# Kernel tuning notes

Measured on AMD Instinct MI355X. Metric: run time of the kernel, lower is better.

## Reference

```python
import jax, jax.numpy as jnp
import numpy as np
from jax import lax

B, N = 16, 4096


def _fps(xyz, npoint):
    # xyz: [N,3] -> [npoint] int32 indices (iterative farthest point sampling, start at idx 0)
    n = xyz.shape[0]
    def step(carry, _):
        dist, far = carry
        d = jnp.sum((xyz - xyz[far]) ** 2, axis=-1)
        dist = jnp.minimum(dist, d)
        nxt = jnp.argmax(dist).astype(jnp.int32)
        return (dist, nxt), far
    (_, _), idx = lax.scan(step, (jnp.full((n,), 1e10, xyz.dtype), jnp.int32(0)), None, length=npoint)
    return idx


def _ball_query(xyz, new_xyz, radius, nsample):
    # xyz: [N,3], new_xyz: [S,3] -> [S, nsample] neighbor indices within radius
    n = xyz.shape[0]
    sqr = jnp.sum((new_xyz[:, None, :] - xyz[None, :, :]) ** 2, axis=-1)  # [S,N]
    idx = jnp.where(sqr > radius * radius, n, jnp.arange(n)[None, :])
    idx = jnp.sort(idx, axis=-1)[:, :nsample]
    return jnp.where(idx == n, idx[:, :1], idx)  # pad misses with first hit


def _gather(p, i):
    return p[i]


def _mlp(feat, ws):
    # feat: [B,S,K,C]; 1x1 conv + folded eval-BN + ReLU per layer
    for W, b in ws:
        feat = jax.nn.relu(jnp.einsum('bskc,oc->bsko', feat, W) + b)
    return feat


def _sa(xyz, points, npoint, radius, nsample, ws):
    fps_idx = jax.vmap(_fps, in_axes=(0, None))(xyz, npoint)              # [B,S]
    new_xyz = jnp.take_along_axis(xyz, fps_idx[..., None], axis=1)         # [B,S,3]
    idx = jax.vmap(_ball_query, in_axes=(0, 0, None, None))(xyz, new_xyz, radius, nsample)  # [B,S,K]
    grouped_xyz = jax.vmap(_gather)(xyz, idx) - new_xyz[:, :, None, :]     # [B,S,K,3]
    if points is None:
        feat = grouped_xyz
    else:
        feat = jnp.concatenate([grouped_xyz, jax.vmap(_gather)(points, idx)], axis=-1)
    return new_xyz, jnp.max(_mlp(feat, ws), axis=2)                        # [B,S,Cout]


def _forward(x, ws1, ws2, ws3, fw, fb):
    b = x.shape[0]
    l1_xyz, l1_pts = _sa(x, None, 512, 0.2, 32, ws1)       # [B,512,3], [B,512,128]
    l2_xyz, l2_pts = _sa(l1_xyz, l1_pts, 128, 0.4, 64, ws2)  # [B,128,3], [B,128,256]
    feat = jnp.concatenate([l2_xyz, l2_pts], axis=-1)[:, None]  # group_all: [B,1,128,259]
    g = jnp.max(_mlp(feat, ws3), axis=2).reshape(b, 1024)
    return g @ fw.T + fb


_SPECS = [
    ('sa1_w0', (64, 3)), ('sa1_b0', (64,)), ('sa1_w1', (64, 64)), ('sa1_b1', (64,)), ('sa1_w2', (128, 64)), ('sa1_b2', (128,)),
    ('sa2_w0', (128, 131)), ('sa2_b0', (128,)), ('sa2_w1', (128, 128)), ('sa2_b1', (128,)), ('sa2_w2', (256, 128)), ('sa2_b2', (256,)),
    ('sa3_w0', (256, 259)), ('sa3_b0', (256,)), ('sa3_w1', (512, 256)), ('sa3_b1', (512,)), ('sa3_w2', (1024, 512)), ('sa3_b2', (1024,)),
    ('fw', (1024, 1024)), ('fb', (1024,)),
]


def setup_inputs() -> dict:
    key = jax.random.key(0)
    keys = jax.random.split(key, len(_SPECS) + 1)
    inp = {'x': jax.random.uniform(keys[0], (B, N, 3), dtype=jnp.float32)}
    for (name, shp), k in zip(_SPECS, keys[1:]):
        inp[name] = jax.random.normal(k, shp, dtype=jnp.float32) * 0.02
    return inp


def reference(x, sa1_w0, sa1_b0, sa1_w1, sa1_b1, sa1_w2, sa1_b2,
              sa2_w0, sa2_b0, sa2_w1, sa2_b1, sa2_w2, sa2_b2,
              sa3_w0, sa3_b0, sa3_w1, sa3_b1, sa3_w2, sa3_b2, fw, fb):
    ws1 = [(sa1_w0, sa1_b0), (sa1_w1, sa1_b1), (sa1_w2, sa1_b2)]
    ws2 = [(sa2_w0, sa2_b0), (sa2_w1, sa2_b1), (sa2_w2, sa2_b2)]
    ws3 = [(sa3_w0, sa3_b0), (sa3_w1, sa3_b1), (sa3_w2, sa3_b2)]
    return _forward(x, ws1, ws2, ws3, fw, fb)
```

## Files before the change

### kernel.cpp

```cpp
#include <hip/hip_runtime.h>

#ifndef BATCH
#define BATCH 16
#endif

typedef float f32x2 __attribute__((ext_vector_type(2)));
__device__ __forceinline__ f32x2 mk2(float a, float b) { f32x2 r; r.x = a; r.y = b; return r; }

template<int CTRL>
__device__ __forceinline__ float dppmaxf(float v)
{
    const int d = __builtin_amdgcn_update_dpp(__float_as_int(v), __float_as_int(v),
                                              CTRL, 0xf, 0xf, false);
    return fmaxf(v, __int_as_float(d));
}
template<int CTRL>
__device__ __forceinline__ unsigned dppminu(unsigned v)
{
    const unsigned d = (unsigned)__builtin_amdgcn_update_dpp((int)v, (int)v,
                                                             CTRL, 0xf, 0xf, false);
    return (d < v) ? d : v;
}
__device__ __forceinline__ float wave_max_bcast(float v)
{
    v = dppmaxf<0x111>(v);
    v = dppmaxf<0x112>(v);
    v = dppmaxf<0x114>(v);
    v = dppmaxf<0x118>(v);
    v = dppmaxf<0x142>(v);
    v = dppmaxf<0x143>(v);
    return __int_as_float(__builtin_amdgcn_readlane(__float_as_int(v), 63));
}
__device__ __forceinline__ unsigned wave_min_bcast(unsigned v)
{
    v = dppminu<0x111>(v);
    v = dppminu<0x112>(v);
    v = dppminu<0x114>(v);
    v = dppminu<0x118>(v);
    v = dppminu<0x142>(v);
    v = dppminu<0x143>(v);
    return (unsigned)__builtin_amdgcn_readlane((int)v, 63);
}

__device__ __forceinline__ void transpose_body(int blk, int tid,
    const float* __restrict__ s0, float* __restrict__ d0,
    const float* __restrict__ s1, float* __restrict__ d1,
    const float* __restrict__ s2, float* __restrict__ d2,
    const float* __restrict__ s3, float* __restrict__ d3,
    const float* __restrict__ s4, float* __restrict__ d4,
    const float* __restrict__ s5, float* __restrict__ d5,
    const float* __restrict__ s6, float* __restrict__ d6,
    const float* __restrict__ s7, float* __restrict__ d7,
    const float* __restrict__ s8, float* __restrict__ d8)
{
    int i = blk * 256 + tid;
    if (i < 192)    { d0[(i%3)  *64   + i/3  ] = s0[i]; return; }  i -= 192;
    if (i < 4096)   { d1[(i&63) *64   + (i>>6)] = s1[i]; return; } i -= 4096;
    if (i < 8192)   { d2[(i&63) *128  + (i>>6)] = s2[i]; return; } i -= 8192;
    if (i < 16768)  { d3[(i%131)*128  + i/131] = s3[i]; return; }  i -= 16768;
    if (i < 16384)  { d4[(i&127)*128  + (i>>7)] = s4[i]; return; } i -= 16384;
    if (i < 32768)  { d5[(i&127)*256  + (i>>7)] = s5[i]; return; } i -= 32768;
    if (i < 66304)  { d6[(i%259)*256  + i/259] = s6[i]; return; }  i -= 66304;
    if (i < 131072) { d7[(i&255)*512  + (i>>8)] = s7[i]; return; } i -= 131072;
    if (i < 524288) { d8[(i&511)*1024 + (i>>9)] = s8[i]; return; }
}

template<int N, int NP1, int NP2, int BLOCK>
__global__ __launch_bounds__(BLOCK)
void fps_fused(const float* __restrict__ xyz,
               float* __restrict__ out1, float* __restrict__ out2,
               const float* __restrict__ ts0, float* __restrict__ td0,
               const float* __restrict__ ts1, float* __restrict__ td1,
               const float* __restrict__ ts2, float* __restrict__ td2,
               const float* __restrict__ ts3, float* __restrict__ td3,
               const float* __restrict__ ts4, float* __restrict__ td4,
               const float* __restrict__ ts5, float* __restrict__ td5,
               const float* __restrict__ ts6, float* __restrict__ td6,
               const float* __restrict__ ts7, float* __restrict__ td7,
               const float* __restrict__ ts8, float* __restrict__ td8)
{
#pragma clang fp contract(off)
    if ((int)blockIdx.x >= BATCH) {
        transpose_body(blockIdx.x - BATCH, threadIdx.x,
                       ts0, td0, ts1, td1, ts2, td2, ts3, td3, ts4, td4,
                       ts5, td5, ts6, td6, ts7, td7, ts8, td8);
        return;
    }
    constexpr int P  = N / BLOCK;
    constexpr int P2 = NP1 / BLOCK;
    constexpr int NW = BLOCK / 64;
    __shared__ float sx[N], sy[N], sz[N];
    __shared__ float s2x[NP1], s2y[NP1], s2z[NP1];
    __shared__ float o2x[NP2], o2y[NP2], o2z[NP2];
    __shared__ unsigned long long wslot[2][NW];
    const int b = blockIdx.x, t = threadIdx.x;
    const int lane = t & 63, wv = t >> 6;
    const float* xb = xyz + (size_t)b * N * 3;
    float px[P], py[P], pz[P], dist[P];
#pragma unroll
    for (int j = 0; j < P; ++j) {
        const int i = t + j * BLOCK;
        const float x = xb[i*3+0], y = xb[i*3+1], z = xb[i*3+2];
        sx[i] = x; sy[i] = y; sz[i] = z;
        px[j] = x; py[j] = y; pz[j] = z;
        dist[j] = 1e10f;
    }
    __syncthreads();
    float fx = sx[0], fy = sy[0], fz = sz[0];
    if (t == 0) { s2x[0] = fx; s2y[0] = fy; s2z[0] = fz; }
    for (int s = 1; s < NP1; ++s) {
        float bestv = -1.f; int besti = 0;
#pragma unroll
        for (int j = 0; j < P; ++j) {
            const float dx = px[j]-fx, dy = py[j]-fy, dz = pz[j]-fz;
            const float d = (dx*dx + dy*dy) + dz*dz;
            const float nd = fminf(dist[j], d);
            dist[j] = nd;
            if (nd > bestv) { bestv = nd; besti = t + j * BLOCK; }
        }
        const float wm = wave_max_bcast(bestv);
        const unsigned cand = (bestv == wm) ? (unsigned)besti : 0xffffffffu;
        const unsigned wi = wave_min_bcast(cand);
        const int par = s & 1;
        if (lane == 0)
            wslot[par][wv] = ((unsigned long long)__float_as_uint(wm) << 32)
                           | (unsigned)(~wi);
        __syncthreads();
        unsigned long long pa = wslot[par][0];
#pragma unroll
        for (int w = 1; w < NW; ++w) {
            const unsigned long long pb = wslot[par][w];
            pa = (pb > pa) ? pb : pa;
        }
        const int far = (int)(~(unsigned)pa);
        fx = sx[far]; fy = sy[far]; fz = sz[far];
        if (t == 0) { s2x[s] = fx; s2y[s] = fy; s2z[s] = fz; }
    }
    __syncthreads();
    float mx[P2], my[P2], mz[P2], d2[P2];
#pragma unroll
    for (int j = 0; j < P2; ++j) {
        const int i = t + j * BLOCK;
        mx[j] = s2x[i]; my[j] = s2y[i]; mz[j] = s2z[i];
        d2[j] = 1e10f;
    }
    fx = s2x[0]; fy = s2y[0]; fz = s2z[0];
    if (t == 0) { o2x[0] = fx; o2y[0] = fy; o2z[0] = fz; }
    for (int s = 1; s < NP2; ++s) {
        float bestv = -1.f; int besti = 0;
#pragma unroll
        for (int j = 0; j < P2; ++j) {
            const float dx = mx[j]-fx, dy = my[j]-fy, dz = mz[j]-fz;
            const float d = (dx*dx + dy*dy) + dz*dz;
            const float nd = fminf(d2[j], d);
            d2[j] = nd;
            if (nd > bestv) { bestv = nd; besti = t + j * BLOCK; }
        }
        const float wm = wave_max_bcast(bestv);
        const unsigned cand = (bestv == wm) ? (unsigned)besti : 0xffffffffu;
        const unsigned wi = wave_min_bcast(cand);
        const int par = s & 1;
        if (lane == 0)
            wslot[par][wv] = ((unsigned long long)__float_as_uint(wm) << 32)
                           | (unsigned)(~wi);
        __syncthreads();
        unsigned long long pa = wslot[par][0];
#pragma unroll
        for (int w = 1; w < NW; ++w) {
            const unsigned long long pb = wslot[par][w];
            pa = (pb > pa) ? pb : pa;
        }
        const int far2 = (int)(~(unsigned)pa);
        fx = s2x[far2]; fy = s2y[far2]; fz = s2z[far2];
        if (t == 0) { o2x[s] = fx; o2y[s] = fy; o2z[s] = fz; }
    }
    __syncthreads();
    for (int i = t; i < NP1; i += BLOCK) {
        out1[((size_t)b*NP1 + i)*3 + 0] = s2x[i];
        out1[((size_t)b*NP1 + i)*3 + 1] = s2y[i];
        out1[((size_t)b*NP1 + i)*3 + 2] = s2z[i];
    }
    for (int i = t; i < NP2; i += BLOCK) {
        out2[((size_t)b*NP2 + i)*3 + 0] = o2x[i];
        out2[((size_t)b*NP2 + i)*3 + 1] = o2y[i];
        out2[((size_t)b*NP2 + i)*3 + 2] = o2z[i];
    }
}

template<int N, int S, int K>
__device__ __forceinline__ void ballq_body(const float* __restrict__ xyz,
                                           const float* __restrict__ nxyz,
                                           int* __restrict__ idx, const float r2,
                                           const int bid, const int tid)
{
#pragma clang fp contract(off)
    const int gw = (bid * 256 + tid) >> 6;
    const int lane = tid & 63;
    const int b = gw / S, s = gw % S;
    const float* xb = xyz + (size_t)b * N * 3;
    const float qx = nxyz[((size_t)b*S + s)*3 + 0];
    const float qy = nxyz[((size_t)b*S + s)*3 + 1];
    const float qz = nxyz[((size_t)b*S + s)*3 + 2];
    int* op = idx + ((size_t)b*S + s) * K;
    int base = 0, first = -1;
    for (int c = 0; c < N; c += 64) {
        const int i = c + lane;
        const float dx = xb[i*3+0]-qx, dy = xb[i*3+1]-qy, dz = xb[i*3+2]-qz;
        const float d = (dx*dx + dy*dy) + dz*dz;
        const bool hit = !(d > r2);
        const unsigned long long m = __ballot(hit);
        if (first < 0 && m) first = c + __builtin_ctzll(m);
        const int pos = base + __popcll(m & ((1ull << lane) - 1ull));
        if (hit && pos < K) op[pos] = i;
        base += __popcll(m);
        if (base >= K) break;
    }
    if (base < K && lane >= base && lane < K) op[lane] = first;
}

__global__ __launch_bounds__(256)
void ballq_both(const float* __restrict__ pts1, const float* __restrict__ q1,
                int* __restrict__ idx1, const float r2a,
                const float* __restrict__ pts2, const float* __restrict__ q2,
                int* __restrict__ idx2, const float r2b)
{
    const int nb1 = (BATCH * 512) / 4;
    if ((int)blockIdx.x < nb1)
        ballq_body<4096, 512, 32>(pts1, q1, idx1, r2a, blockIdx.x, threadIdx.x);
    else
        ballq_body<512, 128, 64>(pts2, q2, idx2, r2b, blockIdx.x - nb1, threadIdx.x);
}

__device__ __forceinline__ void fma16pk(f32x2 (&acc)[8], const float f,
                                        const float* __restrict__ wrow)
{
    const float4 w0 = ((const float4*)wrow)[0];
    const float4 w1 = ((const float4*)wrow)[1];
    const float4 w2 = ((const float4*)wrow)[2];
    const float4 w3 = ((const float4*)wrow)[3];
    const f32x2 ff = mk2(f, f);
    acc[0] += ff * mk2(w0.x, w0.y);
    acc[1] += ff * mk2(w0.z, w0.w);
    acc[2] += ff * mk2(w1.x, w1.y);
    acc[3] += ff * mk2(w1.z, w1.w);
    acc[4] += ff * mk2(w2.x, w2.y);
    acc[5] += ff * mk2(w2.z, w2.w);
    acc[6] += ff * mk2(w3.x, w3.y);
    acc[7] += ff * mk2(w3.z, w3.w);
}

__device__ __forceinline__ float pool_half(float v)
{
    v = fmaxf(v, __shfl_xor(v, 1));
    v = fmaxf(v, __shfl_xor(v, 2));
    v = fmaxf(v, __shfl_xor(v, 4));
    v = fmaxf(v, __shfl_xor(v, 8));
    v = fmaxf(v, __shfl_xor(v, 16));
    return v;
}
__device__ __forceinline__ float pool_full(float v)
{
    v = pool_half(v);
    return fmaxf(v, __shfl_xor(v, 32));
}

__global__ __launch_bounds__(256)
void sa1_fused(const float* __restrict__ xyz, const float* __restrict__ nxyz,
               const int* __restrict__ idx,
               const float* __restrict__ Wt0, const float* __restrict__ B0,
               const float* __restrict__ Wt1, const float* __restrict__ B1,
               const float* __restrict__ Wt2, const float* __restrict__ B2,
               float* __restrict__ out)
{
    __shared__ float buf[64][64];
    const int tid = threadIdx.x, lane = tid & 63;
    const int wave = __builtin_amdgcn_readfirstlane(tid >> 6);
    const int row0 = blockIdx.x * 64;
    const int myrow = row0 + lane;
    const int g = myrow >> 5, b = g >> 9;
    const int i = idx[myrow];
    const float* p = xyz + ((size_t)b*4096 + i) * 3;
    const float f0 = p[0] - nxyz[(size_t)g*3 + 0];
    const float f1 = p[1] - nxyz[(size_t)g*3 + 1];
    const float f2 = p[2] - nxyz[(size_t)g*3 + 2];
    const int oc0 = wave * 16;
    f32x2 aL[8], aH[8];
#pragma unroll
    for (int j = 0; j < 16; ++j) {
        const float v = B0[oc0+j] + f0*Wt0[0*64+oc0+j] + f1*Wt0[1*64+oc0+j] + f2*Wt0[2*64+oc0+j];
        buf[oc0+j][lane] = fmaxf(v, 0.f);
    }
    __syncthreads();
#pragma unroll
    for (int k = 0; k < 8; ++k) aL[k] = mk2(B1[oc0+2*k], B1[oc0+2*k+1]);
#pragma unroll 4
    for (int ci = 0; ci < 64; ++ci)
        fma16pk(aL, buf[ci][lane], Wt1 + ci*64 + oc0);
    __syncthreads();
#pragma unroll
    for (int k = 0; k < 8; ++k) {
        buf[oc0+2*k][lane]   = fmaxf(aL[k].x, 0.f);
        buf[oc0+2*k+1][lane] = fmaxf(aL[k].y, 0.f);
    }
    __syncthreads();
#pragma unroll
    for (int k = 0; k < 8; ++k) {
        aL[k] = mk2(B2[oc0+2*k], B2[oc0+2*k+1]);
        aH[k] = mk2(B2[64+oc0+2*k], B2[64+oc0+2*k+1]);
    }
#pragma unroll 2
    for (int ci = 0; ci < 64; ++ci) {
        const float f = buf[ci][lane];
        fma16pk(aL, f, Wt2 + ci*128 + oc0);
        fma16pk(aH, f, Wt2 + ci*128 + 64 + oc0);
    }
#pragma unroll
    for (int k = 0; k < 8; ++k) {
        const float v0 = pool_half(fmaxf(aL[k].x, 0.f));
        const float v1 = pool_half(fmaxf(aL[k].y, 0.f));
        const float w0 = pool_half(fmaxf(aH[k].x, 0.f));
        const float w1 = pool_half(fmaxf(aH[k].y, 0.f));
        if ((lane & 31) == 0) {
            const size_t orow = (size_t)((row0 + lane) >> 5) * 128;
            out[orow + oc0 + 2*k]       = v0;
            out[orow + oc0 + 2*k + 1]   = v1;
            out[orow + 64 + oc0 + 2*k]     = w0;
            out[orow + 64 + oc0 + 2*k + 1] = w1;
        }
    }
}

__global__ __launch_bounds__(256)
void sa2_fused(const float* __restrict__ l1xyz, const float* __restrict__ l1pts,
               const float* __restrict__ nxyz, const int* __restrict__ idx,
               const float* __restrict__ Wt0, const float* __restrict__ B0,
               const float* __restrict__ Wt1, const float* __restrict__ B1,
               const float* __restrict__ Wt2, const float* __restrict__ B2,
               const float* __restrict__ Wt30, const float* __restrict__ B30,
               float* __restrict__ outH1)
{
    __shared__ float buf[128][64];
    __shared__ float pool[256];
    const int tid = threadIdx.x, lane = tid & 63;
    const int wave = __builtin_amdgcn_readfirstlane(tid >> 6);
    const int gblk = blockIdx.x;
    const int b = gblk >> 7;
    const int row0 = gblk * 64;
    const int myi = idx[row0 + lane];
    const float* pc = l1xyz + ((size_t)b*512 + myi) * 3;
    const float cx = nxyz[(size_t)gblk*3 + 0];
    const float cy = nxyz[(size_t)gblk*3 + 1];
    const float cz = nxyz[(size_t)gblk*3 + 2];
    const float f0 = pc[0] - cx;
    const float f1 = pc[1] - cy;
    const float f2 = pc[2] - cz;
    for (int r = wave; r < 64; r += 4) {
        const int i2 = idx[row0 + r];
        const float* src = l1pts + ((size_t)b*512 + i2) * 128;
        buf[lane][r ^ lane]    = src[lane];
        buf[lane+64][r ^ lane] = src[lane + 64];
    }
    __syncthreads();
    const int oc0 = wave * 16;
    f32x2 aL[8], aH[8];
#pragma unroll
    for (int k = 0; k < 8; ++k) {
        const int j0 = oc0 + 2*k, j1 = oc0 + 2*k + 1;
        aL[k] = mk2(B0[j0]    + f0*Wt0[j0]     + f1*Wt0[128+j0]    + f2*Wt0[256+j0],
                    B0[j1]    + f0*Wt0[j1]     + f1*Wt0[128+j1]    + f2*Wt0[256+j1]);
        aH[k] = mk2(B0[64+j0] + f0*Wt0[64+j0]  + f1*Wt0[192+j0]    + f2*Wt0[320+j0],
                    B0[64+j1] + f0*Wt0[64+j1]  + f1*Wt0[192+j1]    + f2*Wt0[320+j1]);
    }
#pragma unroll 2
    for (int ci = 0; ci < 128; ++ci) {
        const float f = buf[ci][lane ^ (ci & 63)];
        const float* wp = Wt0 + (size_t)(ci+3)*128;
        fma16pk(aL, f, wp + oc0);
        fma16pk(aH, f, wp + 64 + oc0);
    }
    __syncthreads();
#pragma unroll
    for (int k = 0; k < 8; ++k) {
        buf[oc0+2*k][lane]      = fmaxf(aL[k].x, 0.f);
        buf[oc0+2*k+1][lane]    = fmaxf(aL[k].y, 0.f);
        buf[64+oc0+2*k][lane]   = fmaxf(aH[k].x, 0.f);
        buf[64+oc0+2*k+1][lane] = fmaxf(aH[k].y, 0.f);
    }
    __syncthreads();
#pragma unroll
    for (int k = 0; k < 8; ++k) {
        aL[k] = mk2(B1[oc0+2*k], B1[oc0+2*k+1]);
        aH[k] = mk2(B1[64+oc0+2*k], B1[64+oc0+2*k+1]);
    }
#pragma unroll 2
    for (int ci = 0; ci < 128; ++ci) {
        const float f = buf[ci][lane];
        const float* wp = Wt1 + (size_t)ci*128;
        fma16pk(aL, f, wp + oc0);
        fma16pk(aH, f, wp + 64 + oc0);
    }
    __syncthreads();
#pragma unroll
    for (int k = 0; k < 8; ++k) {
        buf[oc0+2*k][lane]      = fmaxf(aL[k].x, 0.f);
        buf[oc0+2*k+1][lane]    = fmaxf(aL[k].y, 0.f);
        buf[64+oc0+2*k][lane]   = fmaxf(aH[k].x, 0.f);
        buf[64+oc0+2*k+1][lane] = fmaxf(aH[k].y, 0.f);
    }
    __syncthreads();
    for (int half = 0; half < 2; ++half) {
        const int oc = half*128 + oc0;
#pragma unroll
        for (int k = 0; k < 8; ++k) {
            aL[k] = mk2(B2[oc+2*k], B2[oc+2*k+1]);
            aH[k] = mk2(B2[64+oc+2*k], B2[64+oc+2*k+1]);
        }
#pragma unroll 2
        for (int ci = 0; ci < 128; ++ci) {
            const float f = buf[ci][lane];
            const float* wp = Wt2 + (size_t)ci*256;
            fma16pk(aL, f, wp + oc);
            fma16pk(aH, f, wp + 64 + oc);
        }
#pragma unroll
        for (int k = 0; k < 8; ++k) {
            const float v0 = pool_full(fmaxf(aL[k].x, 0.f));
            const float v1 = pool_full(fmaxf(aL[k].y, 0.f));
            const float w0 = pool_full(fmaxf(aH[k].x, 0.f));
            const float w1 = pool_full(fmaxf(aH[k].y, 0.f));
            if (lane == 0) {
                pool[oc + 2*k]        = v0;
                pool[oc + 2*k + 1]    = v1;
                pool[64 + oc + 2*k]   = w0;
                pool[64 + oc + 2*k+1] = w1;
            }
        }
    }
    __syncthreads();
    {
        const int oc = tid;
        float acc = B30[oc] + cx*Wt30[0*256+oc] + cy*Wt30[1*256+oc] + cz*Wt30[2*256+oc];
#pragma unroll 8
        for (int ci = 0; ci < 256; ++ci)
            acc += pool[ci] * Wt30[(size_t)(ci+3)*256 + oc];
        outH1[(size_t)gblk*256 + oc] = fmaxf(acc, 0.f);
    }
}

template<int CIN, int COUT, bool CONCAT3, bool POOL>
__global__ __launch_bounds__(256)
void mlp_gemm_kernel(const float* __restrict__ inA, const float* __restrict__ inB,
                     const float* __restrict__ Wt, const float* __restrict__ Bb,
                     float* __restrict__ out)
{
    __shared__ float featS[128][64];
    const int tid = threadIdx.x, lane = tid & 63;
    const int wave = __builtin_amdgcn_readfirstlane(tid >> 6);
    const int row0 = blockIdx.x * 64;
    const int oc0 = blockIdx.y * 64 + wave * 16;
    f32x2 acc[8];
#pragma unroll
    for (int k = 0; k < 8; ++k) acc[k] = mk2(Bb[oc0+2*k], Bb[oc0+2*k+1]);
    for (int c0 = 0; c0 < CIN; c0 += 128) {
        const int csz = (CIN - c0 < 128) ? (CIN - c0) : 128;
        __syncthreads();
        for (int r = wave; r < 64; r += 4) {
            const int row = row0 + r;
            for (int cl = lane; cl < csz; cl += 64) {
                const int cig = c0 + cl;
                float v;
                if (CONCAT3)
                    v = (cig < 3) ? inA[(size_t)row*3 + cig]
                                  : inB[(size_t)row*(CIN-3) + (cig - 3)];
                else
                    v = inA[(size_t)row*CIN + cig];
                featS[cl][r ^ (cl & 63)] = v;
            }
        }
        __syncthreads();
        if (csz == 128) {
#pragma unroll 4
            for (int ci = 0; ci < 128; ++ci)
                fma16pk(acc, featS[ci][lane ^ (ci & 63)], Wt + (size_t)(c0+ci)*COUT + oc0);
        } else {
            for (int ci = 0; ci < csz; ++ci)
                fma16pk(acc, featS[ci][lane ^ (ci & 63)], Wt + (size_t)(c0+ci)*COUT + oc0);
        }
    }
    if (POOL) {
#pragma unroll
        for (int k = 0; k < 8; ++k) {
            const float v0 = pool_full(fmaxf(acc[k].x, 0.f));
            const float v1 = pool_full(fmaxf(acc[k].y, 0.f));
            if (lane == 0) {
                out[(size_t)blockIdx.x * COUT + oc0 + 2*k]     = v0;
                out[(size_t)blockIdx.x * COUT + oc0 + 2*k + 1] = v1;
            }
        }
    } else {
        float4 o0, o1, o2, o3;
        o0.x=fmaxf(acc[0].x,0.f); o0.y=fmaxf(acc[0].y,0.f); o0.z=fmaxf(acc[1].x,0.f); o0.w=fmaxf(acc[1].y,0.f);
        o1.x=fmaxf(acc[2].x,0.f); o1.y=fmaxf(acc[2].y,0.f); o1.z=fmaxf(acc[3].x,0.f); o1.w=fmaxf(acc[3].y,0.f);
        o2.x=fmaxf(acc[4].x,0.f); o2.y=fmaxf(acc[4].y,0.f); o2.z=fmaxf(acc[5].x,0.f); o2.w=fmaxf(acc[5].y,0.f);
        o3.x=fmaxf(acc[6].x,0.f); o3.y=fmaxf(acc[6].y,0.f); o3.z=fmaxf(acc[7].x,0.f); o3.w=fmaxf(acc[7].y,0.f);
        float4* op = (float4*)(out + (size_t)(row0 + lane)*COUT + oc0);
        op[0]=o0; op[1]=o1; op[2]=o2; op[3]=o3;
    }
}

__global__ __launch_bounds__(256)
void fc_kernel(const float* __restrict__ pmax, const float* __restrict__ fw,
               const float* __restrict__ fb, float* __restrict__ y)
{
    const int gw = (blockIdx.x * 256 + threadIdx.x) >> 6;
    const int lane = threadIdx.x & 63;
    const int b = gw >> 10, o = gw & 1023;
    const float4* g0 = (const float4*)(pmax + (size_t)(2*b) * 1024);
    const float4* g1 = (const float4*)(pmax + (size_t)(2*b+1) * 1024);
    const float4* wv = (const float4*)(fw + (size_t)o * 1024);
    float acc = 0.f;
#pragma unroll
    for (int r = 0; r < 4; ++r) {
        const float4 a = g0[lane + r*64];
        const float4 c = g1[lane + r*64];
        const float4 w = wv[lane + r*64];
        acc += fmaxf(a.x,c.x)*w.x + fmaxf(a.y,c.y)*w.y
             + fmaxf(a.z,c.z)*w.z + fmaxf(a.w,c.w)*w.w;
    }
#pragma unroll
    for (int m = 32; m >= 1; m >>= 1) acc += __shfl_xor(acc, m);
    if (lane == 0) y[gw] = acc + fb[o];
}

extern "C" void kernel_launch(void* const* d_in, const int* in_sizes, int n_in,
                              void* d_out, int out_size, void* d_ws, size_t ws_size,
                              hipStream_t stream)
{
    (void)in_sizes; (void)n_in; (void)out_size; (void)ws_size;
    const float* x   = (const float*)d_in[0];
    const float* s1w0 = (const float*)d_in[1];  const float* s1b0 = (const float*)d_in[2];
    const float* s1w1 = (const float*)d_in[3];  const float* s1b1 = (const float*)d_in[4];
    const float* s1w2 = (const float*)d_in[5];  const float* s1b2 = (const float*)d_in[6];
    const float* s2w0 = (const float*)d_in[7];  const float* s2b0 = (const float*)d_in[8];
    const float* s2w1 = (const float*)d_in[9];  const float* s2b1 = (const float*)d_in[10];
    const float* s2w2 = (const float*)d_in[11]; const float* s2b2 = (const float*)d_in[12];
    const float* s3w0 = (const float*)d_in[13]; const float* s3b0 = (const float*)d_in[14];
    const float* s3w1 = (const float*)d_in[15]; const float* s3b1 = (const float*)d_in[16];
    const float* s3w2 = (const float*)d_in[17]; const float* s3b2 = (const float*)d_in[18];
    const float* fw  = (const float*)d_in[19]; const float* fb  = (const float*)d_in[20];
    float* y = (float*)d_out;

    char* ws = (char*)d_ws;
    float* l1_xyz = (float*)(ws + 0);
    int*   idx1   = (int*)  (ws + 98304);
    float* l1_pts = (float*)(ws + 1146880);
    float* l2_xyz = (float*)(ws + 5341184);
    int*   idx2   = (int*)  (ws + 5365760);
    float* h1     = (float*)(ws + 7987200);
    float* h2     = (float*)(ws + 10084352);
    float* pmax   = (float*)(ws + 14278656);
    float* wt1_0  = (float*)(ws + 14409728);
    float* wt1_1  = (float*)(ws + 14410496);
    float* wt1_2  = (float*)(ws + 14426880);
    float* wt2_0  = (float*)(ws + 14459648);
    float* wt2_1  = (float*)(ws + 14526720);
    float* wt2_2  = (float*)(ws + 14592256);
    float* wt3_0  = (float*)(ws + 14723328);
    float* wt3_1  = (float*)(ws + 14988544);
    float* wt3_2  = (float*)(ws + 15512832);

    const float r2_1 = (float)(0.2 * 0.2);
    const float r2_2 = (float)(0.4 * 0.4);

    fps_fused<4096, 512, 128, 256><<<BATCH + 3126, 256, 0, stream>>>(
        x, l1_xyz, l2_xyz,
        s1w0, wt1_0, s1w1, wt1_1, s1w2, wt1_2,
        s2w0, wt2_0, s2w1, wt2_1, s2w2, wt2_2,
        s3w0, wt3_0, s3w1, wt3_1, s3w2, wt3_2);
    ballq_both<<<(BATCH*512)/4 + (BATCH*128)/4, 256, 0, stream>>>(
        x, l1_xyz, idx1, r2_1, l1_xyz, l2_xyz, idx2, r2_2);
    sa1_fused<<<(BATCH*512*32)/64, 256, 0, stream>>>(x, l1_xyz, idx1,
        wt1_0, s1b0, wt1_1, s1b1, wt1_2, s1b2, l1_pts);
    sa2_fused<<<BATCH*128, 256, 0, stream>>>(l1_xyz, l1_pts, l2_xyz, idx2,
        wt2_0, s2b0, wt2_1, s2b1, wt2_2, s2b2, wt3_0, s3b0, h1);
    mlp_gemm_kernel<256, 512,  false, false><<<dim3(32, 8),  256, 0, stream>>>(h1, nullptr, wt3_1, s3b1, h2);
    mlp_gemm_kernel<512, 1024, false, true ><<<dim3(32, 16), 256, 0, stream>>>(h2, nullptr, wt3_2, s3b2, pmax);
    fc_kernel<<<(BATCH*1024)/4, 256, 0, stream>>>(pmax, fw, fb, y);
}
```

Measured before the change: 893.7 us.

## Fuse ball query into SA kernels and fold SA3 layer1 into sa2

Removes the standalone ball-query kernel: each SA1/SA2 block now scans for neighbours itself and keeps the indices in LDS instead of writing them to global memory and reading them back. SA2 also computes the second SA3 MLP layer (256->512) per group, so the separate GEMM launch and the h1 round trip are gone. This saves two launches and some global traffic. In exchange, only 1-2 of the 4 waves do the serial ball-query scan while the others wait at a barrier, and the per-block 256x512 weight pass in sa2 replaces a tiled GEMM.

```diff
diff --git a/kernel.cpp b/kernel.cpp
--- a/kernel.cpp
+++ b/kernel.cpp
@@ -187,21 +187,14 @@
     }
 }
 
-template<int N, int S, int K>
-__device__ __forceinline__ void ballq_body(const float* __restrict__ xyz,
-                                           const float* __restrict__ nxyz,
-                                           int* __restrict__ idx, const float r2,
-                                           const int bid, const int tid)
+template<int N, int K>
+__device__ __forceinline__ void ballq_scan_lds(const float* __restrict__ xb,
+                                               const float qx, const float qy,
+                                               const float qz, const float r2,
+                                               int* __restrict__ sidx,
+                                               const int lane)
 {
 #pragma clang fp contract(off)
-    const int gw = (bid * 256 + tid) >> 6;
-    const int lane = tid & 63;
-    const int b = gw / S, s = gw % S;
-    const float* xb = xyz + (size_t)b * N * 3;
-    const float qx = nxyz[((size_t)b*S + s)*3 + 0];
-    const float qy = nxyz[((size_t)b*S + s)*3 + 1];
-    const float qz = nxyz[((size_t)b*S + s)*3 + 2];
-    int* op = idx + ((size_t)b*S + s) * K;
     int base = 0, first = -1;
     for (int c = 0; c < N; c += 64) {
         const int i = c + lane;
@@ -211,24 +204,11 @@
         const unsigned long long m = __ballot(hit);
         if (first < 0 && m) first = c + __builtin_ctzll(m);
         const int pos = base + __popcll(m & ((1ull << lane) - 1ull));
-        if (hit && pos < K) op[pos] = i;
+        if (hit && pos < K) sidx[pos] = i;
         base += __popcll(m);
         if (base >= K) break;
     }
-    if (base < K && lane >= base && lane < K) op[lane] = first;
-}
-
-__global__ __launch_bounds__(256)
-void ballq_both(const float* __restrict__ pts1, const float* __restrict__ q1,
-                int* __restrict__ idx1, const float r2a,
-                const float* __restrict__ pts2, const float* __restrict__ q2,
-                int* __restrict__ idx2, const float r2b)
-{
-    const int nb1 = (BATCH * 512) / 4;
-    if ((int)blockIdx.x < nb1)
-        ballq_body<4096, 512, 32>(pts1, q1, idx1, r2a, blockIdx.x, threadIdx.x);
-    else
-        ballq_body<512, 128, 64>(pts2, q2, idx2, r2b, blockIdx.x - nb1, threadIdx.x);
+    if (base < K && lane >= base && lane < K) sidx[lane] = first;
 }
 
 __device__ __forceinline__ void fma16pk(f32x2 (&acc)[8], const float f,
@@ -266,20 +246,30 @@
 
 __global__ __launch_bounds__(256)
 void sa1_fused(const float* __restrict__ xyz, const float* __restrict__ nxyz,
-               const int* __restrict__ idx,
+               const float r2,
                const float* __restrict__ Wt0, const float* __restrict__ B0,
                const float* __restrict__ Wt1, const float* __restrict__ B1,
                const float* __restrict__ Wt2, const float* __restrict__ B2,
                float* __restrict__ out)
 {
     __shared__ float buf[64][64];
+    __shared__ int sidx[64];
     const int tid = threadIdx.x, lane = tid & 63;
     const int wave = __builtin_amdgcn_readfirstlane(tid >> 6);
     const int row0 = blockIdx.x * 64;
-    const int myrow = row0 + lane;
-    const int g = myrow >> 5, b = g >> 9;
-    const int i = idx[myrow];
-    const float* p = xyz + ((size_t)b*4096 + i) * 3;
+    const int g0 = row0 >> 5;
+    const int b = g0 >> 9;
+    const float* xb = xyz + (size_t)b * 4096 * 3;
+    if (wave < 2) {
+        const int g = g0 + wave;
+        ballq_scan_lds<4096, 32>(xb,
+            nxyz[(size_t)g*3 + 0], nxyz[(size_t)g*3 + 1], nxyz[(size_t)g*3 + 2],
+            r2, sidx + wave*32, lane);
+    }
+    __syncthreads();
+    const int g = g0 + (lane >> 5);
+    const int i = sidx[lane];
+    const float* p = xb + (size_t)i * 3;
     const float f0 = p[0] - nxyz[(size_t)g*3 + 0];
     const float f1 = p[1] - nxyz[(size_t)g*3 + 1];
     const float f2 = p[2] - nxyz[(size_t)g*3 + 2];
@@ -332,30 +322,36 @@
 
 __global__ __launch_bounds__(256)
 void sa2_fused(const float* __restrict__ l1xyz, const float* __restrict__ l1pts,
-               const float* __restrict__ nxyz, const int* __restrict__ idx,
+               const float* __restrict__ nxyz, const float r2,
                const float* __restrict__ Wt0, const float* __restrict__ B0,
                const float* __restrict__ Wt1, const float* __restrict__ B1,
                const float* __restrict__ Wt2, const float* __restrict__ B2,
                const float* __restrict__ Wt30, const float* __restrict__ B30,
-               float* __restrict__ outH1)
+               const float* __restrict__ Wt31, const float* __restrict__ B31,
+               float* __restrict__ outH2)
 {
     __shared__ float buf[128][64];
     __shared__ float pool[256];
+    __shared__ float h1s[256];
+    __shared__ int sidx[64];
     const int tid = threadIdx.x, lane = tid & 63;
     const int wave = __builtin_amdgcn_readfirstlane(tid >> 6);
     const int gblk = blockIdx.x;
     const int b = gblk >> 7;
-    const int row0 = gblk * 64;
-    const int myi = idx[row0 + lane];
-    const float* pc = l1xyz + ((size_t)b*512 + myi) * 3;
     const float cx = nxyz[(size_t)gblk*3 + 0];
     const float cy = nxyz[(size_t)gblk*3 + 1];
     const float cz = nxyz[(size_t)gblk*3 + 2];
+    const float* xb = l1xyz + (size_t)b * 512 * 3;
+    if (wave == 0)
+        ballq_scan_lds<512, 64>(xb, cx, cy, cz, r2, sidx, lane);
+    __syncthreads();
+    const int myi = sidx[lane];
+    const float* pc = xb + (size_t)myi * 3;
     const float f0 = pc[0] - cx;
     const float f1 = pc[1] - cy;
     const float f2 = pc[2] - cz;
     for (int r = wave; r < 64; r += 4) {
-        const int i2 = idx[row0 + r];
+        const int i2 = sidx[r];
         const float* src = l1pts + ((size_t)b*512 + i2) * 128;
         buf[lane][r ^ lane]    = src[lane];
         buf[lane+64][r ^ lane] = src[lane + 64];
@@ -438,12 +434,23 @@
     }
     __syncthreads();
     {
-        const int oc = tid;
-        float acc = B30[oc] + cx*Wt30[0*256+oc] + cy*Wt30[1*256+oc] + cz*Wt30[2*256+oc];
+        float acc = B30[tid] + cx*Wt30[0*256+tid] + cy*Wt30[1*256+tid] + cz*Wt30[2*256+tid];
 #pragma unroll 8
         for (int ci = 0; ci < 256; ++ci)
-            acc += pool[ci] * Wt30[(size_t)(ci+3)*256 + oc];
-        outH1[(size_t)gblk*256 + oc] = fmaxf(acc, 0.f);
+            acc += pool[ci] * Wt30[(size_t)(ci+3)*256 + tid];
+        h1s[tid] = fmaxf(acc, 0.f);
+    }
+    __syncthreads();
+    {
+        float a0 = B31[tid], a1 = B31[256 + tid];
+#pragma unroll 8
+        for (int ci = 0; ci < 256; ++ci) {
+            const float f = h1s[ci];
+            a0 += f * Wt31[(size_t)ci*512 + tid];
+            a1 += f * Wt31[(size_t)ci*512 + 256 + tid];
+        }
+        outH2[(size_t)gblk*512 + tid]       = fmaxf(a0, 0.f);
+        outH2[(size_t)gblk*512 + 256 + tid] = fmaxf(a1, 0.f);
     }
 }
 
@@ -552,11 +559,8 @@
 
     char* ws = (char*)d_ws;
     float* l1_xyz = (float*)(ws + 0);
-    int*   idx1   = (int*)  (ws + 98304);
     float* l1_pts = (float*)(ws + 1146880);
     float* l2_xyz = (float*)(ws + 5341184);
-    int*   idx2   = (int*)  (ws + 5365760);
-    float* h1     = (float*)(ws + 7987200);
     float* h2     = (float*)(ws + 10084352);
     float* pmax   = (float*)(ws + 14278656);
     float* wt1_0  = (float*)(ws + 14409728);
@@ -577,13 +581,11 @@
         s1w0, wt1_0, s1w1, wt1_1, s1w2, wt1_2,
         s2w0, wt2_0, s2w1, wt2_1, s2w2, wt2_2,
         s3w0, wt3_0, s3w1, wt3_1, s3w2, wt3_2);
-    ballq_both<<<(BATCH*512)/4 + (BATCH*128)/4, 256, 0, stream>>>(
-        x, l1_xyz, idx1, r2_1, l1_xyz, l2_xyz, idx2, r2_2);
-    sa1_fused<<<(BATCH*512*32)/64, 256, 0, stream>>>(x, l1_xyz, idx1,
+    sa1_fused<<<(BATCH*512*32)/64, 256, 0, stream>>>(x, l1_xyz, r2_1,
         wt1_0, s1b0, wt1_1, s1b1, wt1_2, s1b2, l1_pts);
-    sa2_fused<<<BATCH*128, 256, 0, stream>>>(l1_xyz, l1_pts, l2_xyz, idx2,
-        wt2_0, s2b0, wt2_1, s2b1, wt2_2, s2b2, wt3_0, s3b0, h1);
-    mlp_gemm_kernel<256, 512,  false, false><<<dim3(32, 8),  256, 0, stream>>>(h1, nullptr, wt3_1, s3b1, h2);
+    sa2_fused<<<BATCH*128, 256, 0, stream>>>(l1_xyz, l1_pts, l2_xyz, r2_2,
+        wt2_0, s2b0, wt2_1, s2b1, wt2_2, s2b2,
+        wt3_0, s3b0, wt3_1, s3b1, h2);
     mlp_gemm_kernel<512, 1024, false, true ><<<dim3(32, 16), 256, 0, stream>>>(h2, nullptr, wt3_2, s3b2, pmax);
     fc_kernel<<<(BATCH*1024)/4, 256, 0, stream>>>(pmax, fw, fb, y);
 }
```

After: 862.8 us. 1.04x faster.
